# Kernel optimization log

Measured on AMD Instinct MI355X. Metric: run time of the kernel, lower is better.

The kernel has to match this reference:

```python
import jax, jax.numpy as jnp
import numpy as np

B, M, E, NPOS, F, NHEAD, NLAYERS, DFF = 32, 512, 512, 1024, 768, 8, 2, 2048
S = M + 1

def _pe(embed, pad):
    pos = np.arange(pad, dtype=np.float32)[:, None]
    i = np.arange(embed)[None, :]
    ang = pos / np.power(10000.0, (i // 2 * 2.0) / embed)
    pe = np.where(i % 2 == 0, np.sin(ang), np.cos(ang))
    return jnp.asarray(pe, jnp.float32)

PE = _pe(E, M)  # [M, E] sinusoidal table, matches pos_embedding()

def _ln(x, w, b, eps=1e-5):
    mu = x.mean(-1, keepdims=True)
    var = ((x - mu) ** 2).mean(-1, keepdims=True)
    return (x - mu) / jnp.sqrt(var + eps) * w + b

def _mha(x, wi, bi, wo, bo):
    # x: [L, N, E] where L is the attended axis (torch seq dim)
    L, N, Em = x.shape
    Dh = Em // NHEAD
    q, k, v = jnp.split(x @ wi.T + bi, 3, axis=-1)
    q = q.reshape(L, N, NHEAD, Dh) * np.float32(1.0 / np.sqrt(Dh))
    k = k.reshape(L, N, NHEAD, Dh)
    v = v.reshape(L, N, NHEAD, Dh)
    att = jax.nn.softmax(jnp.einsum('lnhd,mnhd->nhlm', q, k), axis=-1)
    o = jnp.einsum('nhlm,mnhd->lnhd', att, v).reshape(L, N, Em)
    return o @ wo.T + bo

def _encoder(x, enc):
    wi, bi, wo, bo, ln1w, ln1b, ln2w, ln2b, w1, b1, w2, b2 = enc
    for l in range(NLAYERS):  # post-norm TransformerEncoderLayer, ReLU, eval mode
        x = _ln(x + _mha(x, wi[l], bi[l], wo[l], bo[l]), ln1w[l], ln1b[l])
        h = jax.nn.relu(x @ w1[l].T + b1[l]) @ w2[l].T + b2[l]
        x = _ln(x + h, ln2w[l], ln2b[l])
    return x

def _forward(pos1, pos2, bert_feature, final_base, emb_table, enc, w_model, w_disc, b_disc):
    emb_table = emb_table.at[0].set(0.0)  # padding_idx=0
    embed = emb_table[pos2] + PE          # [B, M, E]
    starts, ends = pos1[..., 0], pos1[..., 1]
    # loop breaks at first span with end==0: valid = prefix of nonzero ends
    valid = jnp.cumprod((ends != 0).astype(jnp.int32), axis=1).astype(bool)
    k = jnp.arange(M)
    cover = valid[:, :, None] & (starts[:, :, None] <= k) & (k < ends[:, :, None])  # [B, Mspan, Mpos]
    # later spans overwrite earlier ones -> take max covering span index
    span_id = jnp.max(jnp.where(cover, jnp.arange(M)[None, :, None], -1), axis=1)  # [B, Mpos]
    filled = jnp.take_along_axis(embed, jnp.clip(span_id, 0, M - 1)[..., None], axis=1)
    final = jnp.where(span_id[..., None] >= 0, filled, final_base)  # [B, M, E]
    cls = jnp.broadcast_to(emb_table[1], (B, 1, E))
    x = jnp.concatenate([cls, final], axis=1)  # [B, S, E]; torch encoder treats dim0 as seq
    x = _encoder(x, enc)
    pos_feature = jnp.tanh(x @ w_model.T)      # [B, S, F]
    z = jnp.concatenate([bert_feature, pos_feature], axis=-1) @ w_disc.T + b_disc
    return jax.nn.sigmoid(z)                   # [B, S, 1]

def setup_inputs():
    key = jax.random.key(0)
    ks = jax.random.split(key, 12)
    sc = 0.02
    n_valid, chunk = 120, 4  # contiguous spans [4j, 4j+4) for j < 120, then end==0 terminator
    j = np.arange(M)
    starts = np.where(j < n_valid, j * chunk, 0)
    ends = np.where(j < n_valid, j * chunk + chunk, 0)
    pos1 = np.broadcast_to(np.stack([starts, ends], -1), (B, M, 2)).astype(np.int32)
    return {
        'pos1': jnp.asarray(pos1),
        'pos2': jax.random.randint(ks[0], (B, M), 2, NPOS),
        'bert_feature': jax.random.normal(ks[1], (B, S, F), jnp.float32),
        'final_base': jax.random.uniform(ks[2], (B, M, E), jnp.float32),
        'emb_table': jax.random.normal(ks[3], (NPOS, E), jnp.float32) * sc,
        'enc_in_proj_w': jax.random.normal(ks[4], (NLAYERS, 3 * E, E), jnp.float32) * sc,
        'enc_in_proj_b': jnp.zeros((NLAYERS, 3 * E), jnp.float32),
        'enc_out_proj_w': jax.random.normal(ks[5], (NLAYERS, E, E), jnp.float32) * sc,
        'enc_out_proj_b': jnp.zeros((NLAYERS, E), jnp.float32),
        'enc_ln1_w': jnp.ones((NLAYERS, E), jnp.float32),
        'enc_ln1_b': jnp.zeros((NLAYERS, E), jnp.float32),
        'enc_ln2_w': jnp.ones((NLAYERS, E), jnp.float32),
        'enc_ln2_b': jnp.zeros((NLAYERS, E), jnp.float32),
        'enc_ffn_w1': jax.random.normal(ks[6], (NLAYERS, DFF, E), jnp.float32) * sc,
        'enc_ffn_b1': jnp.zeros((NLAYERS, DFF), jnp.float32),
        'enc_ffn_w2': jax.random.normal(ks[7], (NLAYERS, E, DFF), jnp.float32) * sc,
        'enc_ffn_b2': jnp.zeros((NLAYERS, E), jnp.float32),
        'w_model': jax.random.normal(ks[8], (F, E), jnp.float32) * sc,
        'w_disc': jax.random.normal(ks[9], (1, 2 * F), jnp.float32) * sc,
        'b_disc': jnp.zeros((1,), jnp.float32),
    }

def reference(pos1, pos2, bert_feature, final_base, emb_table,
              enc_in_proj_w, enc_in_proj_b, enc_out_proj_w, enc_out_proj_b,
              enc_ln1_w, enc_ln1_b, enc_ln2_w, enc_ln2_b,
              enc_ffn_w1, enc_ffn_b1, enc_ffn_w2, enc_ffn_b2,
              w_model, w_disc, b_disc):
    enc = (enc_in_proj_w, enc_in_proj_b, enc_out_proj_w, enc_out_proj_b,
           enc_ln1_w, enc_ln1_b, enc_ln2_w, enc_ln2_b,
           enc_ffn_w1, enc_ffn_b1, enc_ffn_w2, enc_ffn_b2)
    return _forward(pos1, pos2, bert_feature, final_base, emb_table, enc, w_model, w_disc, b_disc)
```

## Files before the change

### kernel.cpp

```cpp
#include <hip/hip_runtime.h>
#include <hip/hip_bf16.h>

#define B_   32
#define M_   512
#define E_   512
#define S_   513
#define T_   (B_ * S_)
#define TP_  16512
#define NH_  8
#define DH_  64
#define F_   768
#define DFF_ 2048

#define GMT_ 129

typedef short short8 __attribute__((ext_vector_type(8)));
typedef float floatx4 __attribute__((ext_vector_type(4)));

__device__ __forceinline__ float bf2f(unsigned short u) {
    return __uint_as_float(((unsigned int)u) << 16);
}
__device__ __forceinline__ unsigned short f2b_rne(float f) {
    unsigned int u = __float_as_uint(f);
    unsigned int r = u + 0x7FFF + ((u >> 16) & 1);
    return (unsigned short)(r >> 16);
}
__device__ __forceinline__ void gload16(const void* g, void* l) {
    __builtin_amdgcn_global_load_lds(
        (const __attribute__((address_space(1))) void*)g,
        (__attribute__((address_space(3))) void*)l, 16, 0, 0);
}

__global__ void span_kernel(const int* __restrict__ pos1, int* __restrict__ span) {
    int b = blockIdx.x;
    __shared__ int st[M_], en[M_];
    __shared__ int nv;
    int tid = threadIdx.x;
    for (int j = tid; j < M_; j += 256) {
        st[j] = pos1[(b * M_ + j) * 2];
        en[j] = pos1[(b * M_ + j) * 2 + 1];
    }
    __syncthreads();
    if (tid == 0) {
        int n = M_;
        for (int j = 0; j < M_; ++j) if (en[j] == 0) { n = j; break; }
        nv = n;
    }
    __syncthreads();
    int n = nv;
    for (int k = tid; k < M_; k += 256) {
        int best = -1;
        for (int j = 0; j < n; ++j)
            if (st[j] <= k && k < en[j]) best = j;
        span[b * M_ + k] = best;
    }
}

__global__ void f2b5_kernel(const float* __restrict__ s0, const float* __restrict__ s1,
                            const float* __restrict__ s2, const float* __restrict__ s3,
                            const float* __restrict__ s4,
                            unsigned short* __restrict__ dst,
                            int c0, int c1, int c2, int c3, int c4) {
    int i = blockIdx.x * 256 + threadIdx.x;
    if (i >= c4) return;
    float v;
    if      (i < c0) v = s0[i];
    else if (i < c1) v = s1[i - c0];
    else if (i < c2) v = s2[i - c1];
    else if (i < c3) v = s3[i - c2];
    else             v = s4[i - c3];
    dst[i] = f2b_rne(v);
}

__global__ void build_x(const float* __restrict__ emb,
                        const int* __restrict__ pos2,
                        const float* __restrict__ fbase,
                        const int* __restrict__ span,
                        float* __restrict__ x,
                        unsigned short* __restrict__ xb) {
    long long idx = (long long)blockIdx.x * blockDim.x + threadIdx.x;
    if (idx >= (long long)T_ * E_) return;
    int e = (int)(idx % E_);
    int t = (int)(idx / E_);
    int s = t % S_;
    int b = t / S_;
    float val;
    if (s == 0) {
        val = emb[E_ + e];
    } else {
        int k = s - 1;
        int sid = span[b * M_ + k];
        if (sid >= 0) {
            int p = pos2[b * M_ + sid];
            float ex = (float)((e >> 1) << 1) * (1.0f / 512.0f);
            float ang = (float)sid * exp2f(-ex * 13.287712379549449f);
            float pe = (e & 1) ? cosf(ang) : sinf(ang);
            val = emb[(size_t)p * E_ + e] + pe;
        } else {
            val = fbase[((size_t)b * M_ + k) * E_ + e];
        }
    }
    x[idx] = val;
    xb[idx] = f2b_rne(val);
}

template <int ACT, int KT>
__global__ __launch_bounds__(256, 3) void gemm_bf16(const unsigned short* __restrict__ A,
                                                    const unsigned short* __restrict__ W,
                                                    const float* __restrict__ bias,
                                                    unsigned short* __restrict__ Cb,
                                                    int T, int O) {
    constexpr int K = KT;
    constexpr int NSTEP = K / 32;
    __shared__ __align__(16) unsigned short sA[3][128 * 32];
    __shared__ __align__(16) unsigned short sB[3][128 * 32];
    int tid = threadIdx.x;
    int lane = tid & 63, wv = tid >> 6;
    int wr = (wv >> 1) * 64, wc = (wv & 1) * 64;

    int gn = O / 128;
    int per_panel = 8 * gn;
    int id = blockIdx.x;
    int p = id / per_panel;
    int r = id - p * per_panel;
    int mrem = GMT_ - p * 8; if (mrem > 8) mrem = 8;
    int mt = p * 8 + r % mrem;
    int nt = r / mrem;
    int t0 = mt * 128, o0 = nt * 128;

    floatx4 acc[4][4] = {};

    int swz_st = (((lane & 3) ^ ((lane >> 3) & 3))) * 8;
    const unsigned short* Ag = A + (size_t)(t0 + wv * 32 + (lane >> 2)) * K + swz_st;
    const unsigned short* Bg = W + (size_t)(o0 + wv * 32 + (lane >> 2)) * K + swz_st;
    const size_t row16 = (size_t)16 * K;
    const int wvo = wv * 1024;

    int fr = lane & 15;
    int fks = (((lane >> 4) ^ ((lane >> 1) & 3))) * 8;

    auto stage = [&](unsigned short* da, unsigned short* db, int k) {
        gload16(Ag + k, da + wvo);
        gload16(Ag + row16 + k, da + wvo + 512);
        gload16(Bg + k, db + wvo);
        gload16(Bg + row16 + k, db + wvo + 512);
    };
    auto compute = [&](const unsigned short* ca, const unsigned short* cb) {
        short8 af[4], bfr[4];
#pragma unroll
        for (int i = 0; i < 4; ++i)
            af[i] = *(const short8*)&ca[(wr + i * 16 + fr) * 32 + fks];
#pragma unroll
        for (int j = 0; j < 4; ++j)
            bfr[j] = *(const short8*)&cb[(wc + j * 16 + fr) * 32 + fks];
        __builtin_amdgcn_s_setprio(1);
#pragma unroll
        for (int i = 0; i < 4; ++i)
#pragma unroll
            for (int j = 0; j < 4; ++j)
                acc[i][j] = __builtin_amdgcn_mfma_f32_16x16x32_bf16(af[i], bfr[j], acc[i][j], 0, 0, 0);
        __builtin_amdgcn_s_setprio(0);
    };

    unsigned short *a0 = sA[0], *a1 = sA[1], *a2 = sA[2];
    unsigned short *b0 = sB[0], *b1 = sB[1], *b2 = sB[2];

    stage(a0, b0, 0);
    stage(a1, b1, 32);

#pragma unroll 3
    for (int t = 0; t < NSTEP - 2; ++t) {
        asm volatile("s_waitcnt vmcnt(4)" ::: "memory");
        __builtin_amdgcn_s_barrier();
        asm volatile("" ::: "memory");
        stage(a2, b2, (t + 2) * 32);
        compute(a0, b0);
        unsigned short* ta = a0; a0 = a1; a1 = a2; a2 = ta;
        unsigned short* tb = b0; b0 = b1; b1 = b2; b2 = tb;
    }
    asm volatile("s_waitcnt vmcnt(4)" ::: "memory");
    __builtin_amdgcn_s_barrier();
    asm volatile("" ::: "memory");
    compute(a0, b0);
    a0 = a1; b0 = b1;
    asm volatile("s_waitcnt vmcnt(0)" ::: "memory");
    __builtin_amdgcn_s_barrier();
    asm volatile("" ::: "memory");
    compute(a0, b0);

    int cr = (lane >> 4) * 4;
    int cc = lane & 15;
#pragma unroll
    for (int i = 0; i < 4; ++i) {
#pragma unroll
        for (int j = 0; j < 4; ++j) {
            int gn_ = o0 + wc + j * 16 + cc;
            float bv = bias ? bias[gn_] : 0.f;
#pragma unroll
            for (int rr = 0; rr < 4; ++rr) {
                int gm_ = t0 + wr + i * 16 + cr + rr;
                if (gm_ >= T) continue;
                float v = acc[i][j][rr] + bv;
                if (ACT == 1) v = fmaxf(v, 0.f);
                if (ACT == 2) v = tanhf(v);
                Cb[(size_t)gm_ * O + gn_] = f2b_rne(v);
            }
        }
    }
}

__global__ __launch_bounds__(64) void attn_mfma(const unsigned short* __restrict__ qkv,
                                                unsigned short* __restrict__ o) {
    __shared__ __align__(16) unsigned short vt[64 * 40];
    __shared__ __align__(16) unsigned short ps[32 * 40];
    int s = blockIdx.x, h = blockIdx.y;
    int lane = threadIdx.x;
    int hd = h * 64;
    int fr = lane & 15, fq = lane >> 4;

    {
        int m = lane >> 1;
        int d0 = (lane & 1) * 32;
        const unsigned short* vrow = qkv + ((size_t)m * S_ + s) * 1536 + 1024 + hd + d0;
        short8 v0 = *(const short8*)(vrow);
        short8 v1 = *(const short8*)(vrow + 8);
        short8 v2 = *(const short8*)(vrow + 16);
        short8 v3 = *(const short8*)(vrow + 24);
#pragma unroll
        for (int j = 0; j < 8; ++j) {
            vt[(d0 + j) * 40 + m]      = (unsigned short)v0[j];
            vt[(d0 + 8 + j) * 40 + m]  = (unsigned short)v1[j];
            vt[(d0 + 16 + j) * 40 + m] = (unsigned short)v2[j];
            vt[(d0 + 24 + j) * 40 + m] = (unsigned short)v3[j];
        }
    }

    floatx4 c[2][2] = {};
#pragma unroll
    for (int ks = 0; ks < 2; ++ks) {
        short8 aq[2], bk[2];
#pragma unroll
        for (int lt = 0; lt < 2; ++lt) {
            int l = lt * 16 + fr;
            aq[lt] = *(const short8*)(qkv + ((size_t)l * S_ + s) * 1536 + hd + ks * 32 + fq * 8);
        }
#pragma unroll
        for (int mt = 0; mt < 2; ++mt) {
            int m = mt * 16 + fr;
            bk[mt] = *(const short8*)(qkv + ((size_t)m * S_ + s) * 1536 + 512 + hd + ks * 32 + fq * 8);
        }
#pragma unroll
        for (int lt = 0; lt < 2; ++lt)
#pragma unroll
            for (int mt = 0; mt < 2; ++mt)
                c[lt][mt] = __builtin_amdgcn_mfma_f32_16x16x32_bf16(aq[lt], bk[mt], c[lt][mt], 0, 0, 0);
    }

#pragma unroll
    for (int lt = 0; lt < 2; ++lt) {
#pragma unroll
        for (int r = 0; r < 4; ++r) {
            float a = c[lt][0][r] * 0.125f;
            float b = c[lt][1][r] * 0.125f;
            float mx = fmaxf(a, b);
#pragma unroll
            for (int off = 1; off < 16; off <<= 1) mx = fmaxf(mx, __shfl_xor(mx, off));
            float ea = expf(a - mx), eb = expf(b - mx);
            float sm = ea + eb;
#pragma unroll
            for (int off = 1; off < 16; off <<= 1) sm += __shfl_xor(sm, off);
            float inv = 1.f / sm;
            int l = lt * 16 + fq * 4 + r;
            ps[l * 40 + fr]      = f2b_rne(ea * inv);
            ps[l * 40 + 16 + fr] = f2b_rne(eb * inv);
        }
    }
    __syncthreads();

    short8 pa[2], vb[4];
#pragma unroll
    for (int lt = 0; lt < 2; ++lt)
        pa[lt] = *(const short8*)&ps[(lt * 16 + fr) * 40 + fq * 8];
#pragma unroll
    for (int dt = 0; dt < 4; ++dt)
        vb[dt] = *(const short8*)&vt[(dt * 16 + fr) * 40 + fq * 8];

    floatx4 oa[2][4] = {};
#pragma unroll
    for (int lt = 0; lt < 2; ++lt)
#pragma unroll
        for (int dt = 0; dt < 4; ++dt)
            oa[lt][dt] = __builtin_amdgcn_mfma_f32_16x16x32_bf16(pa[lt], vb[dt], oa[lt][dt], 0, 0, 0);

#pragma unroll
    for (int lt = 0; lt < 2; ++lt)
#pragma unroll
        for (int dt = 0; dt < 4; ++dt)
#pragma unroll
            for (int r = 0; r < 4; ++r) {
                int l = lt * 16 + fq * 4 + r;
                o[((size_t)l * S_ + s) * E_ + hd + dt * 16 + fr] = f2b_rne(oa[lt][dt][r]);
            }
}

__global__ __launch_bounds__(256) void add_ln(float* __restrict__ x,
                                              unsigned short* __restrict__ xb,
                                              const unsigned short* __restrict__ h,
                                              const float* __restrict__ w,
                                              const float* __restrict__ b) {
    int t = blockIdx.x;
    float* xr = x + (size_t)t * E_;
    const unsigned short* hr = h + (size_t)t * E_;
    int i0 = threadIdx.x * 2;
    float2 xv = *(const float2*)&xr[i0];
    ushort2 hv = *(const ushort2*)&hr[i0];
    float v0 = xv.x + bf2f(hv.x), v1 = xv.y + bf2f(hv.y);

    __shared__ float red[4];
    float sum = v0 + v1;
    for (int off = 32; off; off >>= 1) sum += __shfl_down(sum, off);
    if ((threadIdx.x & 63) == 0) red[threadIdx.x >> 6] = sum;
    __syncthreads();
    float mu = (red[0] + red[1] + red[2] + red[3]) * (1.0f / E_);
    __syncthreads();

    float d0 = v0 - mu, d1 = v1 - mu;
    float qs = d0 * d0 + d1 * d1;
    for (int off = 32; off; off >>= 1) qs += __shfl_down(qs, off);
    if ((threadIdx.x & 63) == 0) red[threadIdx.x >> 6] = qs;
    __syncthreads();
    float var = (red[0] + red[1] + red[2] + red[3]) * (1.0f / E_);
    float rstd = rsqrtf(var + 1e-5f);

    float o0 = d0 * rstd * w[i0]     + b[i0];
    float o1 = d1 * rstd * w[i0 + 1] + b[i0 + 1];
    *(float2*)&xr[i0] = make_float2(o0, o1);
    xb[(size_t)t * E_ + i0]     = f2b_rne(o0);
    xb[(size_t)t * E_ + i0 + 1] = f2b_rne(o1);
}

__global__ __launch_bounds__(256) void disc_kernel(const float* __restrict__ bert,
                                                   const unsigned short* __restrict__ pf,
                                                   const float* __restrict__ wd,
                                                   const float* __restrict__ bd,
                                                   float* __restrict__ out) {
    int t = blockIdx.x;
    float s = 0.f;
    for (int f = threadIdx.x; f < F_; f += 256) {
        s += bert[(size_t)t * F_ + f] * wd[f];
        s += bf2f(pf[(size_t)t * F_ + f]) * wd[F_ + f];
    }
    for (int off = 32; off; off >>= 1) s += __shfl_down(s, off);
    __shared__ float red[4];
    if ((threadIdx.x & 63) == 0) red[threadIdx.x >> 6] = s;
    __syncthreads();
    if (threadIdx.x == 0) {
        float z = red[0] + red[1] + red[2] + red[3] + bd[0];
        out[t] = 1.f / (1.f + expf(-z));
    }
}

extern "C" void kernel_launch(void* const* d_in, const int* in_sizes, int n_in,
                              void* d_out, int out_size, void* d_ws, size_t ws_size,
                              hipStream_t stream) {
    const int*   pos1 = (const int*)d_in[0];
    const int*   pos2 = (const int*)d_in[1];
    const float* bert = (const float*)d_in[2];
    const float* fb   = (const float*)d_in[3];
    const float* emb  = (const float*)d_in[4];
    const float* wi   = (const float*)d_in[5];
    const float* bi   = (const float*)d_in[6];
    const float* wo   = (const float*)d_in[7];
    const float* bo   = (const float*)d_in[8];
    const float* ln1w = (const float*)d_in[9];
    const float* ln1b = (const float*)d_in[10];
    const float* ln2w = (const float*)d_in[11];
    const float* ln2b = (const float*)d_in[12];
    const float* w1   = (const float*)d_in[13];
    const float* b1   = (const float*)d_in[14];
    const float* w2   = (const float*)d_in[15];
    const float* b2   = (const float*)d_in[16];
    const float* wm   = (const float*)d_in[17];
    const float* wd   = (const float*)d_in[18];
    const float* bd   = (const float*)d_in[19];
    float* out = (float*)d_out;

    float* ws   = (float*)d_ws;
    int*   span = (int*)ws;
    float* x    = ws + 16384;
    unsigned short* xb  = (unsigned short*)(x + (size_t)T_ * 512);
    unsigned short* atb = xb + (size_t)TP_ * 512;
    unsigned short* hb  = atb + (size_t)TP_ * 512;
    unsigned short* U   = hb + (size_t)T_ * 512;
    unsigned short* qkvb = U;
    unsigned short* h1b  = U;
    unsigned short* pfb  = U;
    unsigned short* wib  = U + (size_t)TP_ * 2048;
    const int NWI = 2 * 1536 * 512;
    const int NWO = 2 * 512 * 512;
    const int NW1 = 2 * 2048 * 512;
    const int NW2 = 2 * 512 * 2048;
    const int NWM = 768 * 512;
    unsigned short* wob = wib + NWI;
    unsigned short* w1b = wob + NWO;
    unsigned short* w2b = w1b + NW1;
    unsigned short* wmb = w2b + NW2;

    span_kernel<<<B_, 256, 0, stream>>>(pos1, span);
    {
        int c0 = NWI, c1 = c0 + NWO, c2 = c1 + NW1, c3 = c2 + NW2, c4 = c3 + NWM;
        f2b5_kernel<<<(c4 + 255) / 256, 256, 0, stream>>>(wi, wo, w1, w2, wm, wib,
                                                          c0, c1, c2, c3, c4);
    }
    build_x<<<(int)(((long long)T_ * 512 + 255) / 256), 256, 0, stream>>>(emb, pos2, fb, span, x, xb);

    for (int l = 0; l < 2; ++l) {
        gemm_bf16<0, 512><<<GMT_ * (1536 / 128), 256, 0, stream>>>(
            xb, wib + (size_t)l * 1536 * 512, bi + l * 1536, qkvb, T_, 1536);
        attn_mfma<<<dim3(S_, NH_), 64, 0, stream>>>(qkvb, atb);
        gemm_bf16<0, 512><<<GMT_ * (512 / 128), 256, 0, stream>>>(
            atb, wob + (size_t)l * 512 * 512, bo + l * 512, hb, T_, 512);
        add_ln<<<T_, 256, 0, stream>>>(x, xb, hb, ln1w + l * 512, ln1b + l * 512);
        gemm_bf16<1, 512><<<GMT_ * (2048 / 128), 256, 0, stream>>>(
            xb, w1b + (size_t)l * 2048 * 512, b1 + l * 2048, h1b, T_, 2048);
        gemm_bf16<0, 2048><<<GMT_ * (512 / 128), 256, 0, stream>>>(
            h1b, w2b + (size_t)l * 512 * 2048, b2 + l * 512, hb, T_, 512);
        add_ln<<<T_, 256, 0, stream>>>(x, xb, hb, ln2w + l * 512, ln2b + l * 512);
    }
    gemm_bf16<2, 512><<<GMT_ * (768 / 128), 256, 0, stream>>>(
        xb, wmb, nullptr, pfb, T_, 768);
    disc_kernel<<<T_, 256, 0, stream>>>(bert, pfb, wd, bd, out);
}
```

Measured before the change: 780.6 us.

## Enlarge GEMM tile to 256x128 with double-buffered LDS pipeline

Changes the bf16 GEMM block tile from 128x128 to 256x128, with each wave computing a 128x64 sub-tile (8x4 MFMA accumulators). This raises the ratio of MFMA work to LDS fragment loads. The LDS pipeline goes from triple to double buffering, with an extra barrier before the next stage is issued, and occupancy is lowered to 2 blocks per CU. The grid shrinks to 65 M-tiles, so the last tile is heavily padded, fewer blocks are available to fill the CUs, and register pressure rises.

```diff
diff --git a/kernel.cpp b/kernel.cpp
--- a/kernel.cpp
+++ b/kernel.cpp
@@ -12,7 +12,7 @@
 #define F_   768
 #define DFF_ 2048
 
-#define GMT_ 129
+#define GM2_ 65
 
 typedef short short8 __attribute__((ext_vector_type(8)));
 typedef float floatx4 __attribute__((ext_vector_type(4)));
@@ -105,93 +105,94 @@
 }
 
 template <int ACT, int KT>
-__global__ __launch_bounds__(256, 3) void gemm_bf16(const unsigned short* __restrict__ A,
+__global__ __launch_bounds__(256, 2) void gemm_bf16(const unsigned short* __restrict__ A,
                                                     const unsigned short* __restrict__ W,
                                                     const float* __restrict__ bias,
                                                     unsigned short* __restrict__ Cb,
                                                     int T, int O) {
     constexpr int K = KT;
     constexpr int NSTEP = K / 32;
-    __shared__ __align__(16) unsigned short sA[3][128 * 32];
-    __shared__ __align__(16) unsigned short sB[3][128 * 32];
+    __shared__ __align__(16) unsigned short sA[2][256 * 32];
+    __shared__ __align__(16) unsigned short sB[2][128 * 32];
     int tid = threadIdx.x;
     int lane = tid & 63, wv = tid >> 6;
-    int wr = (wv >> 1) * 64, wc = (wv & 1) * 64;
+    int wr = (wv >> 1) * 128, wc = (wv & 1) * 64;
 
     int gn = O / 128;
     int per_panel = 8 * gn;
     int id = blockIdx.x;
     int p = id / per_panel;
     int r = id - p * per_panel;
-    int mrem = GMT_ - p * 8; if (mrem > 8) mrem = 8;
+    int mrem = GM2_ - p * 8; if (mrem > 8) mrem = 8;
     int mt = p * 8 + r % mrem;
     int nt = r / mrem;
-    int t0 = mt * 128, o0 = nt * 128;
-
-    floatx4 acc[4][4] = {};
-
-    int swz_st = (((lane & 3) ^ ((lane >> 3) & 3))) * 8;
-    const unsigned short* Ag = A + (size_t)(t0 + wv * 32 + (lane >> 2)) * K + swz_st;
-    const unsigned short* Bg = W + (size_t)(o0 + wv * 32 + (lane >> 2)) * K + swz_st;
-    const size_t row16 = (size_t)16 * K;
-    const int wvo = wv * 1024;
+    int t0 = mt * 256, o0 = nt * 128;
+
+    floatx4 acc[8][4] = {};
+
+    int swz_st = ((lane & 3) ^ ((lane >> 3) & 3)) * 8;
+    const unsigned short* Ag = A + (size_t)(t0 + wv * 16 + (lane >> 2)) * K + swz_st;
+    const unsigned short* Bg = W + (size_t)(o0 + wv * 16 + (lane >> 2)) * K + swz_st;
+    const size_t rstride = (size_t)64 * K;
 
     int fr = lane & 15;
-    int fks = (((lane >> 4) ^ ((lane >> 1) & 3))) * 8;
+    int fks = ((lane >> 4) ^ ((lane >> 1) & 3)) * 8;
 
     auto stage = [&](unsigned short* da, unsigned short* db, int k) {
-        gload16(Ag + k, da + wvo);
-        gload16(Ag + row16 + k, da + wvo + 512);
-        gload16(Bg + k, db + wvo);
-        gload16(Bg + row16 + k, db + wvo + 512);
+#pragma unroll
+        for (int rr = 0; rr < 4; ++rr)
+            gload16(Ag + k + rr * rstride, da + (rr * 4 + wv) * 512);
+#pragma unroll
+        for (int rr = 0; rr < 2; ++rr)
+            gload16(Bg + k + rr * rstride, db + (rr * 4 + wv) * 512);
     };
     auto compute = [&](const unsigned short* ca, const unsigned short* cb) {
-        short8 af[4], bfr[4];
-#pragma unroll
-        for (int i = 0; i < 4; ++i)
+        short8 af[8];
+#pragma unroll
+        for (int i = 0; i < 8; ++i)
             af[i] = *(const short8*)&ca[(wr + i * 16 + fr) * 32 + fks];
-#pragma unroll
-        for (int j = 0; j < 4; ++j)
-            bfr[j] = *(const short8*)&cb[(wc + j * 16 + fr) * 32 + fks];
         __builtin_amdgcn_s_setprio(1);
 #pragma unroll
-        for (int i = 0; i < 4; ++i)
-#pragma unroll
-            for (int j = 0; j < 4; ++j)
-                acc[i][j] = __builtin_amdgcn_mfma_f32_16x16x32_bf16(af[i], bfr[j], acc[i][j], 0, 0, 0);
+        for (int j = 0; j < 4; ++j) {
+            short8 bf = *(const short8*)&cb[(wc + j * 16 + fr) * 32 + fks];
+#pragma unroll
+            for (int i = 0; i < 8; ++i)
+                acc[i][j] = __builtin_amdgcn_mfma_f32_16x16x32_bf16(af[i], bf, acc[i][j], 0, 0, 0);
+        }
         __builtin_amdgcn_s_setprio(0);
     };
 
-    unsigned short *a0 = sA[0], *a1 = sA[1], *a2 = sA[2];
-    unsigned short *b0 = sB[0], *b1 = sB[1], *b2 = sB[2];
+    unsigned short *a0 = sA[0], *a1 = sA[1];
+    unsigned short *b0 = sB[0], *b1 = sB[1];
 
     stage(a0, b0, 0);
     stage(a1, b1, 32);
 
-#pragma unroll 3
+#pragma unroll 2
     for (int t = 0; t < NSTEP - 2; ++t) {
-        asm volatile("s_waitcnt vmcnt(4)" ::: "memory");
+        asm volatile("s_waitcnt vmcnt(6)" ::: "memory");
         __builtin_amdgcn_s_barrier();
         asm volatile("" ::: "memory");
-        stage(a2, b2, (t + 2) * 32);
         compute(a0, b0);
-        unsigned short* ta = a0; a0 = a1; a1 = a2; a2 = ta;
-        unsigned short* tb = b0; b0 = b1; b1 = b2; b2 = tb;
-    }
-    asm volatile("s_waitcnt vmcnt(4)" ::: "memory");
+        __builtin_amdgcn_s_barrier();
+        asm volatile("" ::: "memory");
+        stage(a0, b0, (t + 2) * 32);
+        unsigned short* ta = a0; a0 = a1; a1 = ta;
+        unsigned short* tb = b0; b0 = b1; b1 = tb;
+    }
+    asm volatile("s_waitcnt vmcnt(6)" ::: "memory");
     __builtin_amdgcn_s_barrier();
     asm volatile("" ::: "memory");
     compute(a0, b0);
-    a0 = a1; b0 = b1;
     asm volatile("s_waitcnt vmcnt(0)" ::: "memory");
     __builtin_amdgcn_s_barrier();
     asm volatile("" ::: "memory");
-    compute(a0, b0);
+    compute(a1, b1);
 
     int cr = (lane >> 4) * 4;
     int cc = lane & 15;
 #pragma unroll
-    for (int i = 0; i < 4; ++i) {
+    for (int i = 0; i < 8; ++i) {
 #pragma unroll
         for (int j = 0; j < 4; ++j) {
             int gn_ = o0 + wc + j * 16 + cc;
@@ -415,19 +416,19 @@
     build_x<<<(int)(((long long)T_ * 512 + 255) / 256), 256, 0, stream>>>(emb, pos2, fb, span, x, xb);
 
     for (int l = 0; l < 2; ++l) {
-        gemm_bf16<0, 512><<<GMT_ * (1536 / 128), 256, 0, stream>>>(
+        gemm_bf16<0, 512><<<GM2_ * (1536 / 128), 256, 0, stream>>>(
             xb, wib + (size_t)l * 1536 * 512, bi + l * 1536, qkvb, T_, 1536);
         attn_mfma<<<dim3(S_, NH_), 64, 0, stream>>>(qkvb, atb);
-        gemm_bf16<0, 512><<<GMT_ * (512 / 128), 256, 0, stream>>>(
+        gemm_bf16<0, 512><<<GM2_ * (512 / 128), 256, 0, stream>>>(
             atb, wob + (size_t)l * 512 * 512, bo + l * 512, hb, T_, 512);
         add_ln<<<T_, 256, 0, stream>>>(x, xb, hb, ln1w + l * 512, ln1b + l * 512);
-        gemm_bf16<1, 512><<<GMT_ * (2048 / 128), 256, 0, stream>>>(
+        gemm_bf16<1, 512><<<GM2_ * (2048 / 128), 256, 0, stream>>>(
             xb, w1b + (size_t)l * 2048 * 512, b1 + l * 2048, h1b, T_, 2048);
-        gemm_bf16<0, 2048><<<GMT_ * (512 / 128), 256, 0, stream>>>(
+        gemm_bf16<0, 2048><<<GM2_ * (512 / 128), 256, 0, stream>>>(
             h1b, w2b + (size_t)l * 512 * 2048, b2 + l * 512, hb, T_, 512);
         add_ln<<<T_, 256, 0, stream>>>(x, xb, hb, ln2w + l * 512, ln2b + l * 512);
     }
-    gemm_bf16<2, 512><<<GMT_ * (768 / 128), 256, 0, stream>>>(
+    gemm_bf16<2, 512><<<GM2_ * (768 / 128), 256, 0, stream>>>(
         xb, wmb, nullptr, pfb, T_, 768);
     disc_kernel<<<T_, 256, 0, stream>>>(bert, pfb, wd, bd, out);
 }
```

Result: slower. 888.1 us (+13.8%).
